# Kernel tuning notes

Hardware: AMD Instinct MI355X
Metric: run time of the kernel (lower is better)

The kernel has to match this reference:

```python
import jax, jax.numpy as jnp
import numpy as np

B, T, C = 4, 1024, 1024
H, D = 16, 64  # num_heads, head_channels
EPS = 1e-5


def layernorm(x, g, b):
    mu = jnp.mean(x, axis=-1, keepdims=True)
    d = x - mu
    var = jnp.mean(d * d, axis=-1, keepdims=True)
    return d * jax.lax.rsqrt(var + EPS) * g + b


def setup_inputs() -> dict:
    key = jax.random.key(0)
    ks = jax.random.split(key, 5)
    s = 0.02  # init scale for weights
    return {
        "x": jax.random.normal(ks[0], (B, T, C), jnp.float32),
        "norm_g": jnp.ones((C,), jnp.float32),
        "norm_b": jnp.zeros((C,), jnp.float32),
        "qkv_w": jax.random.normal(ks[1], (C, 3 * C), jnp.float32) * s,
        "qkv_b": jax.random.normal(ks[2], (3 * C,), jnp.float32) * s,
        "qln_g": jnp.ones((C,), jnp.float32),
        "qln_b": jnp.zeros((C,), jnp.float32),
        "kln_g": jnp.ones((C,), jnp.float32),
        "kln_b": jnp.zeros((C,), jnp.float32),
        "proj_w": jax.random.normal(ks[3], (C, C), jnp.float32) * s,
        "proj_b": jax.random.normal(ks[4], (C,), jnp.float32) * s,
    }


def reference(x, norm_g, norm_b, qkv_w, qkv_b, qln_g, qln_b, kln_g, kln_b, proj_w, proj_b):
    in_dtype = x.dtype
    # pre-LN computed in fp32, cast back to input dtype
    xn = layernorm(x.astype(jnp.float32), norm_g, norm_b).astype(in_dtype)
    qkv = xn @ qkv_w + qkv_b  # [B,T,3C]
    q, k, v = jnp.split(qkv, 3, axis=-1)
    # per-Q/K LayerNorm over the full channel dim (before head split)
    q = layernorm(q, qln_g, qln_b)
    k = layernorm(k, kln_g, kln_b)
    # [B,T,C] -> [B,H,T,D]
    to_heads = lambda t: t.reshape(B, T, H, D).transpose(0, 2, 1, 3)
    q, k, v = to_heads(q), to_heads(k), to_heads(v)
    temp = 1.0
    scale = (D ** -0.5) / temp  # sqrt_scale**2 / temp
    scores = jnp.einsum("bhqd,bhkd->bhqk", q, k) * scale
    attn = jax.nn.softmax(scores, axis=-1)
    out = jnp.einsum("bhqk,bhkd->bhqd", attn, v)
    out = out.transpose(0, 2, 1, 3).reshape(B, T, C)
    return out @ proj_w + proj_b
```

## Files before the change

### kernel.cpp

```cpp
#include <hip/hip_runtime.h>
#include <math.h>

#define T_SEQ 1024
#define C_DIM 1024
#define NB    4
#define NH    16
#define HD    64
#define C3    3072

typedef __attribute__((ext_vector_type(8))) short bf16x8;
typedef __attribute__((ext_vector_type(4))) float f32x4;
typedef unsigned short u16;

union B8 { bf16x8 v; u16 u[8]; unsigned d[4]; };

__device__ inline u16 bf16_rtn(float v) {
    unsigned int u = __float_as_uint(v);
    u += 0x7FFFu + ((u >> 16) & 1u);
    return (u16)(u >> 16);
}
__device__ inline void split_bf16(float v, u16& hi, u16& lo) {
    hi = bf16_rtn(v);
    float hif = __uint_as_float(((unsigned int)hi) << 16);
    lo = bf16_rtn(v - hif);
}

__global__ __launch_bounds__(256) void ln_split_kernel(const float* __restrict__ in,
                                                       u16* __restrict__ oh,
                                                       u16* __restrict__ ol,
                                                       const float* __restrict__ g,
                                                       const float* __restrict__ beta) {
    const int row = blockIdx.x;
    const float* x = in + (size_t)row * 1024;
    const int t = threadIdx.x;

    float4 v = *(const float4*)&x[t * 4];
    float s  = v.x + v.y + v.z + v.w;
    float ss = v.x * v.x + v.y * v.y + v.z * v.z + v.w * v.w;
    #pragma unroll
    for (int m = 1; m < 64; m <<= 1) {
        s  += __shfl_xor(s, m);
        ss += __shfl_xor(ss, m);
    }
    __shared__ float red[8];
    const int wave = t >> 6, lane = t & 63;
    if (lane == 0) { red[wave * 2] = s; red[wave * 2 + 1] = ss; }
    __syncthreads();
    s  = red[0] + red[2] + red[4] + red[6];
    ss = red[1] + red[3] + red[5] + red[7];

    const float mu   = s * (1.0f / 1024.0f);
    const float var  = ss * (1.0f / 1024.0f) - mu * mu;
    const float rstd = rsqrtf(var + 1e-5f);

    float4 gg = *(const float4*)&g[t * 4];
    float4 bb = *(const float4*)&beta[t * 4];
    float o[4];
    o[0] = (v.x - mu) * rstd * gg.x + bb.x;
    o[1] = (v.y - mu) * rstd * gg.y + bb.y;
    o[2] = (v.z - mu) * rstd * gg.z + bb.z;
    o[3] = (v.w - mu) * rstd * gg.w + bb.w;

    ushort4 h4, l4;
    split_bf16(o[0], h4.x, l4.x);
    split_bf16(o[1], h4.y, l4.y);
    split_bf16(o[2], h4.z, l4.z);
    split_bf16(o[3], h4.w, l4.w);
    size_t off = (size_t)row * 1024 + t * 4;
    *(ushort4*)&oh[off] = h4;
    *(ushort4*)&ol[off] = l4;
}

__global__ __launch_bounds__(256) void ln_qk_kernel(float* __restrict__ qkv,
                                                    const float* __restrict__ qg,
                                                    const float* __restrict__ qb,
                                                    const float* __restrict__ kg,
                                                    const float* __restrict__ kb,
                                                    u16* __restrict__ Kh,
                                                    u16* __restrict__ Kl) {
    const int row = blockIdx.x;
    const int isK = row >> 12;
    const int r = row & 4095;
    float* x = qkv + (size_t)r * C3 + (isK ? 1024 : 0);
    const float* g    = isK ? kg : qg;
    const float* beta = isK ? kb : qb;
    const int t = threadIdx.x;

    float4 v = *(const float4*)&x[t * 4];
    float s  = v.x + v.y + v.z + v.w;
    float ss = v.x * v.x + v.y * v.y + v.z * v.z + v.w * v.w;
    #pragma unroll
    for (int m = 1; m < 64; m <<= 1) {
        s  += __shfl_xor(s, m);
        ss += __shfl_xor(ss, m);
    }
    __shared__ float red[8];
    const int wave = t >> 6, lane = t & 63;
    if (lane == 0) { red[wave * 2] = s; red[wave * 2 + 1] = ss; }
    __syncthreads();
    s  = red[0] + red[2] + red[4] + red[6];
    ss = red[1] + red[3] + red[5] + red[7];

    const float mu   = s * (1.0f / 1024.0f);
    const float var  = ss * (1.0f / 1024.0f) - mu * mu;
    const float rstd = rsqrtf(var + 1e-5f);

    float4 gg = *(const float4*)&g[t * 4];
    float4 bb = *(const float4*)&beta[t * 4];
    float o0 = (v.x - mu) * rstd * gg.x + bb.x;
    float o1 = (v.y - mu) * rstd * gg.y + bb.y;
    float o2 = (v.z - mu) * rstd * gg.z + bb.z;
    float o3 = (v.w - mu) * rstd * gg.w + bb.w;

    if (!isK) {
        float4 o = {o0, o1, o2, o3};
        *(float4*)&x[t * 4] = o;
    } else {
        ushort4 h4, l4;
        split_bf16(o0, h4.x, l4.x);
        split_bf16(o1, h4.y, l4.y);
        split_bf16(o2, h4.z, l4.z);
        split_bf16(o3, h4.w, l4.w);
        const int c = t * 4;
        const int hh = c >> 6, d = c & 63;
        const int b = r >> 10, tt = r & 1023;
        size_t off = ((size_t)((b << 4) + hh) << 16) + (size_t)tt * 64 + d;
        *(ushort4*)&Kh[off] = h4;
        *(ushort4*)&Kl[off] = l4;
    }
}

__global__ __launch_bounds__(256) void vsplit_t(const float* __restrict__ qkv,
                                                u16* __restrict__ Vth,
                                                u16* __restrict__ Vtl) {
    __shared__ float tile[64][68];
    const int bid = blockIdx.x;
    const int tt = bid & 15, h = (bid >> 4) & 15, b = bid >> 8;
    const int t = threadIdx.x;
    const float* src = qkv + (size_t)(b * 1024 + tt * 64) * C3 + 2048 + h * 64;
    #pragma unroll
    for (int i = 0; i < 4; ++i) {
        int idx = i * 256 + t;
        int tr = idx >> 4, dc = (idx & 15) * 4;
        float4 v = *(const float4*)&src[(size_t)tr * C3 + dc];
        tile[tr][dc + 0] = v.x; tile[tr][dc + 1] = v.y;
        tile[tr][dc + 2] = v.z; tile[tr][dc + 3] = v.w;
    }
    __syncthreads();
    #pragma unroll
    for (int i = 0; i < 4; ++i) {
        int idx = i * 256 + t;
        int d = idx >> 4, tc = (idx & 15) * 4;
        ushort4 h4, l4;
        split_bf16(tile[tc + 0][d], h4.x, l4.x);
        split_bf16(tile[tc + 1][d], h4.y, l4.y);
        split_bf16(tile[tc + 2][d], h4.z, l4.z);
        split_bf16(tile[tc + 3][d], h4.w, l4.w);
        size_t off = ((size_t)((b * 16 + h) * 64 + d)) * 1024 + tt * 64 + tc;
        *(ushort4*)&Vth[off] = h4;
        *(ushort4*)&Vtl[off] = l4;
    }
}

__global__ __launch_bounds__(256) void wsplit_t(const float* __restrict__ W,
                                                u16* __restrict__ Th,
                                                u16* __restrict__ Tl,
                                                int K, int N, int ldt) {
    __shared__ float tile[64][69];
    const int n0 = blockIdx.x * 64, k0 = blockIdx.y * 64;
    const int t = threadIdx.x;
    #pragma unroll
    for (int i = 0; i < 4; ++i) {
        int idx = t + 256 * i;
        int kr = idx >> 4, nc = (idx & 15) * 4;
        float4 v = *(const float4*)&W[(size_t)(k0 + kr) * N + n0 + nc];
        tile[kr][nc + 0] = v.x; tile[kr][nc + 1] = v.y;
        tile[kr][nc + 2] = v.z; tile[kr][nc + 3] = v.w;
    }
    __syncthreads();
    #pragma unroll
    for (int i = 0; i < 4; ++i) {
        int idx = t + 256 * i;
        int nr = idx >> 4, kc = (idx & 15) * 4;
        ushort4 h4, l4;
        split_bf16(tile[kc + 0][nr], h4.x, l4.x);
        split_bf16(tile[kc + 1][nr], h4.y, l4.y);
        split_bf16(tile[kc + 2][nr], h4.z, l4.z);
        split_bf16(tile[kc + 3][nr], h4.w, l4.w);
        size_t o = (size_t)(n0 + nr) * ldt + k0 + kc;
        *(ushort4*)&Th[o] = h4;
        *(ushort4*)&Tl[o] = l4;
    }
}

__global__ __launch_bounds__(256) void gemm_mfma_split(
    const u16* __restrict__ Ah, const u16* __restrict__ Al,
    const u16* __restrict__ Bh, const u16* __restrict__ Bl,
    const float* __restrict__ bias, float* __restrict__ C,
    int M, int N, int K, int lda, int ldb) {
    __shared__ u16 sAh[128 * 32], sAl[128 * 32], sBh[128 * 32], sBl[128 * 32];

    const int t    = threadIdx.x;
    const int lane = t & 63;
    const int wid  = t >> 6;
    const int wr   = wid >> 1, wc = wid & 1;

    const int nbx = gridDim.x;
    const int nwg = nbx * gridDim.y;
    int bid = blockIdx.y * nbx + blockIdx.x;
    int swz = (bid & 7) * (nwg >> 3) + (bid >> 3);
    const int bn = (swz % nbx) * 128;
    const int bm = (swz / nbx) * 128;

    const int jr    = lane >> 2;
    const int cphys = lane & 3;
    const int m16 = lane & 15, g8 = lane >> 4;

    f32x4 acc[4][4];
    #pragma unroll
    for (int m = 0; m < 4; ++m)
        #pragma unroll
        for (int n = 0; n < 4; ++n) {
            f32x4 z = {0.0f, 0.0f, 0.0f, 0.0f};
            acc[m][n] = z;
        }

    for (int k0 = 0; k0 < K; k0 += 32) {
        __syncthreads();
        #pragma unroll
        for (int jj = 0; jj < 2; ++jj) {
            const int j = wid * 2 + jj;
            const int r = (j << 4) + jr;
            const int cl = cphys ^ (r & 3);
            const size_t ga = ((size_t)(bm + r) * lda + k0 + (cl << 3)) * 2;
            const size_t gb = ((size_t)(bn + r) * ldb + k0 + (cl << 3)) * 2;
            const unsigned ldso = (unsigned)(j << 10);
            __builtin_amdgcn_global_load_lds(
                (const __attribute__((address_space(1))) void*)((const char*)Ah + ga),
                (__attribute__((address_space(3))) void*)((char*)sAh + ldso), 16, 0, 0);
            __builtin_amdgcn_global_load_lds(
                (const __attribute__((address_space(1))) void*)((const char*)Al + ga),
                (__attribute__((address_space(3))) void*)((char*)sAl + ldso), 16, 0, 0);
            __builtin_amdgcn_global_load_lds(
                (const __attribute__((address_space(1))) void*)((const char*)Bh + gb),
                (__attribute__((address_space(3))) void*)((char*)sBh + ldso), 16, 0, 0);
            __builtin_amdgcn_global_load_lds(
                (const __attribute__((address_space(1))) void*)((const char*)Bl + gb),
                (__attribute__((address_space(3))) void*)((char*)sBl + ldso), 16, 0, 0);
        }
        __syncthreads();

        bf16x8 ah[4], al[4], bh[4], bl[4];
        #pragma unroll
        for (int m = 0; m < 4; ++m) {
            const int r = wr * 64 + m * 16 + m16;
            const int off = (r << 5) + ((g8 ^ (m16 & 3)) << 3);
            ah[m] = *(const bf16x8*)&sAh[off];
            al[m] = *(const bf16x8*)&sAl[off];
        }
        #pragma unroll
        for (int n = 0; n < 4; ++n) {
            const int r = wc * 64 + n * 16 + m16;
            const int off = (r << 5) + ((g8 ^ (m16 & 3)) << 3);
            bh[n] = *(const bf16x8*)&sBh[off];
            bl[n] = *(const bf16x8*)&sBl[off];
        }
        #pragma unroll
        for (int m = 0; m < 4; ++m)
            #pragma unroll
            for (int n = 0; n < 4; ++n) {
                acc[m][n] = __builtin_amdgcn_mfma_f32_16x16x32_bf16(ah[m], bh[n], acc[m][n], 0, 0, 0);
                acc[m][n] = __builtin_amdgcn_mfma_f32_16x16x32_bf16(al[m], bh[n], acc[m][n], 0, 0, 0);
                acc[m][n] = __builtin_amdgcn_mfma_f32_16x16x32_bf16(ah[m], bl[n], acc[m][n], 0, 0, 0);
            }
    }

    #pragma unroll
    for (int m = 0; m < 4; ++m) {
        const int row0 = bm + wr * 64 + m * 16 + (g8 << 2);
        #pragma unroll
        for (int n = 0; n < 4; ++n) {
            const int col = bn + wc * 64 + n * 16 + m16;
            const float bv = bias[col];
            #pragma unroll
            for (int e = 0; e < 4; ++e)
                C[(size_t)(row0 + e) * N + col] = acc[m][n][e] + bv;
        }
    }
}

__global__ __launch_bounds__(256) void attn_mfma(const float* __restrict__ qkv,
                                                 const u16* __restrict__ Kh,
                                                 const u16* __restrict__ Kl,
                                                 const u16* __restrict__ Vth,
                                                 const u16* __restrict__ Vtl,
                                                 u16* __restrict__ att) {
    __shared__ __align__(16) u16 SM[32768];

    const int t    = threadIdx.x;
    const int lane = t & 63;
    const int wv   = t >> 6;
    const int m16  = lane & 15, g8 = lane >> 4;

    const int bid  = blockIdx.x;
    const int work = (bid & 7) * 128 + (bid >> 3);
    const int qt = work & 15;
    const int bh = work >> 4;
    const int h  = bh & 15;
    const int b  = bh >> 4;
    const int q0 = qt * 64;

    const int srow = lane >> 3;
    const int scl  = (lane & 7) ^ srow;
    const size_t kvrow0 = (size_t)bh << 16;

    auto stageK = [&](int kt) {
        const int kb = kt * 64;
        #pragma unroll
        for (int issue = 0; issue < 2; ++issue) {
            const int rloc = (issue * 4 + wv) * 8 + srow;
            const size_t go = (kvrow0 + (size_t)(kb + rloc) * 64 + scl * 8) * 2;
            const unsigned lo = (unsigned)((issue * 4 + wv) * 1024);
            __builtin_amdgcn_global_load_lds(
                (const __attribute__((address_space(1))) void*)((const char*)Kh + go),
                (__attribute__((address_space(3))) void*)((char*)SM + lo), 16, 0, 0);
            __builtin_amdgcn_global_load_lds(
                (const __attribute__((address_space(1))) void*)((const char*)Kl + go),
                (__attribute__((address_space(3))) void*)((char*)SM + 8192 + lo), 16, 0, 0);
        }
    };
    auto stageV = [&](int kt, int bsel) {
        const int kb = kt * 64;
        #pragma unroll
        for (int issue = 0; issue < 2; ++issue) {
            const int rloc = (issue * 4 + wv) * 8 + srow;
            const size_t go = (kvrow0 + (size_t)rloc * 1024 + kb + scl * 8) * 2;
            const unsigned lo = (unsigned)(16384 + bsel * 16384 + (issue * 4 + wv) * 1024);
            __builtin_amdgcn_global_load_lds(
                (const __attribute__((address_space(1))) void*)((const char*)Vth + go),
                (__attribute__((address_space(3))) void*)((char*)SM + lo), 16, 0, 0);
            __builtin_amdgcn_global_load_lds(
                (const __attribute__((address_space(1))) void*)((const char*)Vtl + go),
                (__attribute__((address_space(3))) void*)((char*)SM + 8192 + lo), 16, 0, 0);
        }
    };

    bf16x8 qh[2], ql[2];
    {
        const float* qrow = qkv + (size_t)(b * T_SEQ + q0 + wv * 16 + m16) * C3 + h * HD;
        #pragma unroll
        for (int ds = 0; ds < 2; ++ds) {
            float4 a = *(const float4*)&qrow[ds * 32 + g8 * 8];
            float4 c = *(const float4*)&qrow[ds * 32 + g8 * 8 + 4];
            float q8[8] = {a.x, a.y, a.z, a.w, c.x, c.y, c.z, c.w};
            B8 hh, ll;
            #pragma unroll
            for (int j = 0; j < 8; ++j) {
                u16 hi, lo;
                split_bf16(q8[j] * 0.125f, hi, lo);
                hh.u[j] = hi; ll.u[j] = lo;
            }
            qh[ds] = hh.v; ql[ds] = ll.v;
        }
    }

    f32x4 acc_o[4];
    #pragma unroll
    for (int i = 0; i < 4; ++i) { f32x4 z = {0, 0, 0, 0}; acc_o[i] = z; }
    float m_run = -INFINITY, l_run = 0.0f;

    u16* Phw = SM + 24576 + wv * 1024;
    u16* Plw = SM + 28672 + wv * 1024;

    stageK(0);
    stageV(0, 0);
    asm volatile("s_waitcnt vmcnt(0)" ::: "memory");
    __builtin_amdgcn_s_barrier();
    __builtin_amdgcn_sched_barrier(0);

    int vsel = 0;
    for (int kt = 0; kt < 16; ++kt) {
        f32x4 accs[4];
        #pragma unroll
        for (int i = 0; i < 4; ++i) { f32x4 z = {0, 0, 0, 0}; accs[i] = z; }
        #pragma unroll
        for (int ds = 0; ds < 2; ++ds) {
            #pragma unroll
            for (int sub = 0; sub < 4; ++sub) {
                const int row = sub * 16 + m16;
                const int idx = row * 64 + ((((ds * 4 + g8)) ^ (m16 & 7)) << 3);
                bf16x8 kh = *(const bf16x8*)&SM[idx];
                bf16x8 kl = *(const bf16x8*)&SM[4096 + idx];
                accs[sub] = __builtin_amdgcn_mfma_f32_16x16x32_bf16(kh, qh[ds], accs[sub], 0, 0, 0);
                accs[sub] = __builtin_amdgcn_mfma_f32_16x16x32_bf16(kl, qh[ds], accs[sub], 0, 0, 0);
                accs[sub] = __builtin_amdgcn_mfma_f32_16x16x32_bf16(kh, ql[ds], accs[sub], 0, 0, 0);
            }
        }

        __builtin_amdgcn_sched_barrier(0);
        __builtin_amdgcn_s_barrier();
        __builtin_amdgcn_sched_barrier(0);
        if (kt < 15) { stageK(kt + 1); stageV(kt + 1, vsel ^ 1); }

        float mt = accs[0][0];
        #pragma unroll
        for (int sub = 0; sub < 4; ++sub)
            #pragma unroll
            for (int e = 0; e < 4; ++e) mt = fmaxf(mt, accs[sub][e]);
        mt = fmaxf(mt, __shfl_xor(mt, 16));
        mt = fmaxf(mt, __shfl_xor(mt, 32));
        const float mnew = fmaxf(m_run, mt);
        const float fsc = __expf(m_run - mnew);
        float p[4][4];
        float ts = 0.0f;
        #pragma unroll
        for (int sub = 0; sub < 4; ++sub)
            #pragma unroll
            for (int e = 0; e < 4; ++e) {
                p[sub][e] = __expf(accs[sub][e] - mnew);
                ts += p[sub][e];
            }
        ts += __shfl_xor(ts, 16);
        ts += __shfl_xor(ts, 32);
        l_run = l_run * fsc + ts;
        m_run = mnew;
        #pragma unroll
        for (int d = 0; d < 4; ++d)
            #pragma unroll
            for (int e = 0; e < 4; ++e) acc_o[d][e] *= fsc;

        #pragma unroll
        for (int sub = 0; sub < 4; ++sub)
            #pragma unroll
            for (int pp = 0; pp < 2; ++pp) {
                float p0 = p[sub][2 * pp], p1 = p[sub][2 * pp + 1];
                u16 h0, l0, h1, l1;
                split_bf16(p0, h0, l0);
                split_bf16(p1, h1, l1);
                unsigned hw = (unsigned)h0 | ((unsigned)h1 << 16);
                unsigned lw = (unsigned)l0 | ((unsigned)l1 << 16);
                const int idx = m16 * 64 + (((2 * sub + (g8 >> 1)) ^ (m16 & 7)) << 3)
                                + 4 * (g8 & 1) + 2 * pp;
                *(unsigned*)&Phw[idx] = hw;
                *(unsigned*)&Plw[idx] = lw;
            }

        bf16x8 pfh[2], pfl[2];
        #pragma unroll
        for (int ks = 0; ks < 2; ++ks) {
            const int idx = m16 * 64 + ((((ks * 4 + g8)) ^ (m16 & 7)) << 3);
            pfh[ks] = *(const bf16x8*)&Phw[idx];
            pfl[ks] = *(const bf16x8*)&Plw[idx];
        }

        const int vb = 8192 + vsel * 8192;
        #pragma unroll
        for (int dsub = 0; dsub < 4; ++dsub) {
            #pragma unroll
            for (int ks = 0; ks < 2; ++ks) {
                const int vrow = dsub * 16 + m16;
                const int vidx = vb + vrow * 64 + ((((ks * 4 + g8)) ^ (m16 & 7)) << 3);
                bf16x8 vh = *(const bf16x8*)&SM[vidx];
                bf16x8 vl = *(const bf16x8*)&SM[4096 + vidx];
                acc_o[dsub] = __builtin_amdgcn_mfma_f32_16x16x32_bf16(vh, pfh[ks], acc_o[dsub], 0, 0, 0);
                acc_o[dsub] = __builtin_amdgcn_mfma_f32_16x16x32_bf16(vh, pfl[ks], acc_o[dsub], 0, 0, 0);
                acc_o[dsub] = __builtin_amdgcn_mfma_f32_16x16x32_bf16(vl, pfh[ks], acc_o[dsub], 0, 0, 0);
            }
        }

        __builtin_amdgcn_sched_barrier(0);
        asm volatile("s_waitcnt vmcnt(0)" ::: "memory");
        __builtin_amdgcn_s_barrier();
        __builtin_amdgcn_sched_barrier(0);
        vsel ^= 1;
    }

    const float linv = 1.0f / l_run;
    #pragma unroll
    for (int dsub = 0; dsub < 4; ++dsub)
        #pragma unroll
        for (int pp = 0; pp < 2; ++pp) {
            float o0 = acc_o[dsub][2 * pp] * linv;
            float o1 = acc_o[dsub][2 * pp + 1] * linv;
            u16 h0, l0, h1, l1;
            split_bf16(o0, h0, l0);
            split_bf16(o1, h1, l1);
            unsigned hw = (unsigned)h0 | ((unsigned)h1 << 16);
            unsigned lw = (unsigned)l0 | ((unsigned)l1 << 16);
            const int idx = m16 * 64 + (((2 * dsub + (g8 >> 1)) ^ (m16 & 7)) << 3)
                            + 4 * (g8 & 1) + 2 * pp;
            *(unsigned*)&Phw[idx] = hw;
            *(unsigned*)&Plw[idx] = lw;
        }
    __syncthreads();
    #pragma unroll
    for (int i = 0; i < 2; ++i) {
        int s = t + 256 * i;
        int q_l = s >> 3, dg8 = s & 7;
        const int idx = q_l * 64 + ((dg8 ^ (q_l & 7)) << 3);
        bf16x8 oh = *(const bf16x8*)&SM[24576 + idx];
        bf16x8 ol = *(const bf16x8*)&SM[28672 + idx];
        size_t off = (size_t)(b * T_SEQ + q0 + q_l) * 6144 + 2048 + h * HD + dg8 * 8;
        *(bf16x8*)&att[off] = oh;
        *(bf16x8*)&att[off + 1024] = ol;
    }
}

extern "C" void kernel_launch(void* const* d_in, const int* in_sizes, int n_in,
                              void* d_out, int out_size, void* d_ws, size_t ws_size,
                              hipStream_t stream) {
    const float* x      = (const float*)d_in[0];
    const float* norm_g = (const float*)d_in[1];
    const float* norm_b = (const float*)d_in[2];
    const float* qkv_w  = (const float*)d_in[3];
    const float* qkv_b  = (const float*)d_in[4];
    const float* qln_g  = (const float*)d_in[5];
    const float* qln_b  = (const float*)d_in[6];
    const float* kln_g  = (const float*)d_in[7];
    const float* kln_b  = (const float*)d_in[8];
    const float* proj_w = (const float*)d_in[9];
    const float* proj_b = (const float*)d_in[10];
    float* out = (float*)d_out;

    char* w = (char*)d_ws;
    float* qkv    = (float*)w;
    u16* qkv_u16  = (u16*)w;
    u16* xn_hi    = (u16*)(w + 50331648);
    u16* xn_lo    = (u16*)(w + 58720256);
    u16* wq_hi    = (u16*)(w + 67108864);
    u16* wq_lo    = (u16*)(w + 73400320);
    u16* Kh       = xn_hi;
    u16* Kl       = xn_lo;
    u16* Vth      = (u16*)(w + 67108864);
    u16* Vtl      = (u16*)(w + 75497472);
    u16* pw_hi    = qkv_u16 + 4096;
    u16* pw_lo    = qkv_u16 + 5120;
    u16* att_hi   = qkv_u16 + 2048;
    u16* att_lo   = qkv_u16 + 3072;

    const int rows = NB * T_SEQ;

    ln_split_kernel<<<rows, 256, 0, stream>>>(x, xn_hi, xn_lo, norm_g, norm_b);
    wsplit_t<<<dim3(C3 / 64, C_DIM / 64), 256, 0, stream>>>(qkv_w, wq_hi, wq_lo, C_DIM, C3, 1024);
    gemm_mfma_split<<<dim3(C3 / 128, rows / 128), 256, 0, stream>>>(
        xn_hi, xn_lo, wq_hi, wq_lo, qkv_b, qkv, rows, C3, C_DIM, 1024, 1024);
    ln_qk_kernel<<<2 * rows, 256, 0, stream>>>(qkv, qln_g, qln_b, kln_g, kln_b, Kh, Kl);
    vsplit_t<<<1024, 256, 0, stream>>>(qkv, Vth, Vtl);
    wsplit_t<<<dim3(C_DIM / 64, C_DIM / 64), 256, 0, stream>>>(proj_w, pw_hi, pw_lo, C_DIM, C_DIM, 6144);
    attn_mfma<<<1024, 256, 0, stream>>>(qkv, Kh, Kl, Vth, Vtl, qkv_u16);
    gemm_mfma_split<<<dim3(C_DIM / 128, rows / 128), 256, 0, stream>>>(
        att_hi, att_lo, pw_hi, pw_lo, proj_b, out, rows, C_DIM, C_DIM, 6144, 6144);
}
```

Before: 337.3 us.

## Add 256x256-tile split-bf16 GEMM with direct global-to-LDS loads for QKV projection

```diff
diff --git a/kernel.cpp b/kernel.cpp
--- a/kernel.cpp
+++ b/kernel.cpp
@@ -193,6 +193,121 @@
     }
 }
 
+__global__ __launch_bounds__(512, 2) void gemm256_mfma_split(
+    const u16* __restrict__ Ah, const u16* __restrict__ Al,
+    const u16* __restrict__ Bh, const u16* __restrict__ Bl,
+    const float* __restrict__ bias, float* __restrict__ C,
+    int N, int lda, int ldb) {
+    __shared__ __align__(16) u16 SM[65536];
+
+    const int t    = threadIdx.x;
+    const int lane = t & 63;
+    const int wid  = t >> 6;
+    const int wr   = wid >> 2;
+    const int wc   = wid & 3;
+    const int m16  = lane & 15, g8 = lane >> 4;
+
+    const int nbx = gridDim.x;
+    const int nwg = nbx * gridDim.y;
+    int bid = blockIdx.y * nbx + blockIdx.x;
+    int swz = (bid & 7) * (nwg >> 3) + (bid >> 3);
+    const int bn = (swz % nbx) * 256;
+    const int bm = (swz / nbx) * 256;
+
+    f32x4 acc[8][4];
+    #pragma unroll
+    for (int m = 0; m < 8; ++m)
+        #pragma unroll
+        for (int n = 0; n < 4; ++n) {
+            f32x4 z = {0.0f, 0.0f, 0.0f, 0.0f};
+            acc[m][n] = z;
+        }
+
+    auto STAGE = [&](int tile, int buf) {
+        const int reg = tile >> 4;
+        const u16* Ab = (reg == 1) ? Al : Ah;
+        const u16* Bb = (reg == 2) ? Bl : Bh;
+        const int kloc = (tile & 15) << 6;
+        #pragma unroll
+        for (int i = 0; i < 4; ++i) {
+            const int idx = i * 512 + t;
+            const int r = idx >> 3;
+            const int cl = (idx & 7) ^ (r & 7);
+            const size_t ga = ((size_t)(bm + r) * lda + kloc + cl * 8) * 2;
+            const size_t gb = ((size_t)(bn + r) * ldb + kloc + cl * 8) * 2;
+            const unsigned la = (unsigned)(buf * 32768 + idx * 16);
+            const unsigned lb = (unsigned)(65536 + buf * 32768 + idx * 16);
+            __builtin_amdgcn_global_load_lds(
+                (const __attribute__((address_space(1))) void*)((const char*)Ab + ga),
+                (__attribute__((address_space(3))) void*)((char*)SM + la), 16, 0, 0);
+            __builtin_amdgcn_global_load_lds(
+                (const __attribute__((address_space(1))) void*)((const char*)Bb + gb),
+                (__attribute__((address_space(3))) void*)((char*)SM + lb), 16, 0, 0);
+        }
+    };
+
+    STAGE(0, 0);
+    STAGE(1, 1);
+    asm volatile("s_waitcnt vmcnt(8)" ::: "memory");
+    __builtin_amdgcn_s_barrier();
+    __builtin_amdgcn_sched_barrier(0);
+
+    for (int tt = 0; tt < 48; ++tt) {
+        const int cb = tt & 1;
+        const u16* Abuf = SM + cb * 16384;
+        const u16* Bbuf = SM + 32768 + cb * 16384;
+
+        bf16x8 bf[4][2];
+        #pragma unroll
+        for (int n = 0; n < 4; ++n)
+            #pragma unroll
+            for (int ks = 0; ks < 2; ++ks) {
+                const int r = wc * 64 + n * 16 + m16;
+                bf[n][ks] = *(const bf16x8*)&Bbuf[r * 64 + (((ks * 4 + g8) ^ (r & 7)) << 3)];
+            }
+        __builtin_amdgcn_s_setprio(1);
+        #pragma unroll
+        for (int m = 0; m < 8; ++m) {
+            const int r = wr * 128 + m * 16 + m16;
+            bf16x8 a0 = *(const bf16x8*)&Abuf[r * 64 + ((g8 ^ (r & 7)) << 3)];
+            bf16x8 a1 = *(const bf16x8*)&Abuf[r * 64 + (((4 + g8) ^ (r & 7)) << 3)];
+            #pragma unroll
+            for (int n = 0; n < 4; ++n) {
+                acc[m][n] = __builtin_amdgcn_mfma_f32_16x16x32_bf16(a0, bf[n][0], acc[m][n], 0, 0, 0);
+                acc[m][n] = __builtin_amdgcn_mfma_f32_16x16x32_bf16(a1, bf[n][1], acc[m][n], 0, 0, 0);
+            }
+        }
+        __builtin_amdgcn_s_setprio(0);
+
+        __builtin_amdgcn_sched_barrier(0);
+        __builtin_amdgcn_s_barrier();
+        __builtin_amdgcn_sched_barrier(0);
+        if (tt + 2 < 48) {
+            STAGE(tt + 2, cb);
+            __builtin_amdgcn_sched_barrier(0);
+            asm volatile("s_waitcnt vmcnt(8)" ::: "memory");
+        } else {
+            asm volatile("s_waitcnt vmcnt(0)" ::: "memory");
+        }
+        __builtin_amdgcn_sched_barrier(0);
+        __builtin_amdgcn_s_barrier();
+        __builtin_amdgcn_sched_barrier(0);
+    }
+
+    #pragma unroll
+    for (int m = 0; m < 8; ++m) {
+        const int row0 = bm + wr * 128 + m * 16 + (g8 << 2);
+        #pragma unroll
+        for (int n = 0; n < 4; ++n) {
+            const int col = bn + wc * 64 + n * 16 + m16;
+            const float bv = bias[col];
+            #pragma unroll
+            for (int e = 0; e < 4; ++e)
+                C[(size_t)(row0 + e) * N + col] = acc[m][n][e] + bv;
+        }
+    }
+}
+
 __global__ __launch_bounds__(256) void gemm_mfma_split(
     const u16* __restrict__ Ah, const u16* __restrict__ Al,
     const u16* __restrict__ Bh, const u16* __restrict__ Bl,
@@ -542,8 +657,8 @@
 
     ln_split_kernel<<<rows, 256, 0, stream>>>(x, xn_hi, xn_lo, norm_g, norm_b);
     wsplit_t<<<dim3(C3 / 64, C_DIM / 64), 256, 0, stream>>>(qkv_w, wq_hi, wq_lo, C_DIM, C3, 1024);
-    gemm_mfma_split<<<dim3(C3 / 128, rows / 128), 256, 0, stream>>>(
-        xn_hi, xn_lo, wq_hi, wq_lo, qkv_b, qkv, rows, C3, C_DIM, 1024, 1024);
+    gemm256_mfma_split<<<dim3(C3 / 256, rows / 256), 512, 0, stream>>>(
+        xn_hi, xn_lo, wq_hi, wq_lo, qkv_b, qkv, C3, 1024, 1024);
     ln_qk_kernel<<<2 * rows, 256, 0, stream>>>(qkv, qln_g, qln_b, kln_g, kln_b, Kh, Kl);
     vsplit_t<<<1024, 256, 0, stream>>>(qkv, Vth, Vtl);
     wsplit_t<<<dim3(C_DIM / 64, C_DIM / 64), 256, 0, stream>>>(proj_w, pw_hi, pw_lo, C_DIM, C_DIM, 6144);
```

Measured after the change: 330.5 us. 2.0% less time.
